# Performance work log

Hardware: AMD Instinct MI355X
Metric: run time of the kernel (lower is better)

## Reference

```python
import jax, jax.numpy as jnp
import numpy as np

NG, NT, E = 2500, 20000, 640000
SRC_DIM, DST_DIM, HID, OUT, NCLS = 128, 500, 128, 128, 16


def setup_inputs() -> dict:
    key = jax.random.key(0)
    ks = jax.random.split(key, 11)
    d = {
        "gene_feats": jax.random.normal(ks[0], (NG, SRC_DIM), jnp.float32),
        "train_feats": jax.random.normal(ks[1], (NT, DST_DIM), jnp.float32),
        "edge_src": jax.random.randint(ks[2], (E,), 0, NG),
        "edge_dst": jax.random.randint(ks[3], (E,), 0, NT),
        # conv1: SAGEConv((src_dim, dst_dim) -> hidden)
        "W1_neigh": jax.random.normal(ks[4], (SRC_DIM, HID), jnp.float32) / np.sqrt(SRC_DIM),
        "W1_self": jax.random.normal(ks[5], (DST_DIM, HID), jnp.float32) / np.sqrt(DST_DIM),
        "b1": jnp.zeros((HID,), jnp.float32),
        # conv2: SAGEConv(hidden -> out); src input is the raw gene features
        "W2_neigh": jax.random.normal(ks[6], (HID, OUT), jnp.float32) / np.sqrt(HID),
        "W2_self": jax.random.normal(ks[7], (HID, OUT), jnp.float32) / np.sqrt(HID),
        "b2": jnp.zeros((OUT,), jnp.float32),
        # classifier MLP
        "Wc1": jax.random.normal(ks[8], (OUT, OUT), jnp.float32) / np.sqrt(OUT),
        "bc1": jnp.zeros((OUT,), jnp.float32),
        "Wc2": jax.random.normal(ks[9], (OUT, NCLS), jnp.float32) / np.sqrt(OUT),
        "bc2": jnp.zeros((NCLS,), jnp.float32),
    }
    return d


def _segment_mean(msgs, dst, num_segments):
    # mean over in-edges; isolated dst nodes get 0 (DGL convention)
    sums = jax.ops.segment_sum(msgs, dst, num_segments=num_segments)
    cnt = jax.ops.segment_sum(jnp.ones((msgs.shape[0],), msgs.dtype), dst,
                              num_segments=num_segments)
    return sums / jnp.maximum(cnt, 1.0)[:, None]


def reference(gene_feats, train_feats, edge_src, edge_dst,
              W1_neigh, W1_self, b1, W2_neigh, W2_self, b2,
              Wc1, bc1, Wc2, bc2):
    # mean-aggregate gene (src) features onto train (dst) nodes
    agg = _segment_mean(gene_feats[edge_src], edge_dst, NT)  # [NT, SRC_DIM]
    # conv1: fc_self(h_dst) + fc_neigh(mean_neigh) + bias, then ReLU
    h1 = jax.nn.relu(train_feats @ W1_self + agg @ W1_neigh + b1)  # [NT, HID]
    # conv2 reuses raw gene features as src -> same mean aggregation
    h2 = jax.nn.relu(h1 @ W2_self + agg @ W2_neigh + b2)  # [NT, OUT]
    # classifier: Linear -> ReLU -> Linear
    return jax.nn.relu(h2 @ Wc1 + bc1) @ Wc2 + bc2  # [NT, NCLS]
```

## Files before the change

### kernel.cpp

```cpp
#include <hip/hip_runtime.h>


#define NG 2500
#define NT 20000
#define NE 640000
#define NCLS 16
#define CAP 96
#define NTILE 1250

typedef unsigned short u16;
typedef unsigned int u32;

typedef float f32x4 __attribute__((ext_vector_type(4)));
typedef __bf16 bf16x8 __attribute__((ext_vector_type(8)));

__device__ __forceinline__ float b2f(u16 u) { return __uint_as_float(((u32)u) << 16); }
__device__ __forceinline__ float blo(u32 p) { return __uint_as_float(p << 16); }
__device__ __forceinline__ float bhi(u32 p) { return __uint_as_float(p & 0xffff0000u); }
__device__ __forceinline__ u16 f2b(float f) {
    u32 u = __float_as_uint(f);
    return (u16)((u + 0x7fffu + ((u >> 16) & 1u)) >> 16);
}

#define B1N 81920
#define B2N 32768
#define B3N 16384
#define B4N 2048
#define NEB 2500
#define CVB NTILE
#define GNB 625
#define PKB 520

__global__ __launch_bounds__(256) void k_prep(
    const int* __restrict__ esrc, const int* __restrict__ edst,
    int* __restrict__ cnt, u16* __restrict__ csr,
    const float* __restrict__ train, const float* __restrict__ gene,
    u16* __restrict__ AF, u32* __restrict__ GH32,
    const float* __restrict__ W1n, const float* __restrict__ W1s,
    const float* __restrict__ W2n, const float* __restrict__ W2s,
    const float* __restrict__ Wc1, const float* __restrict__ Wc2,
    u16* __restrict__ B1h, u16* __restrict__ B1l,
    u16* __restrict__ B2h, u16* __restrict__ B2l,
    u16* __restrict__ B3h, u16* __restrict__ B3l,
    u16* __restrict__ B4h, u16* __restrict__ B4l) {
    int blk = blockIdx.x, t = threadIdx.x;
    if (blk < NEB) {
        int e = blk * 256 + t;
        if (e < NE) {
            unsigned d = (unsigned)edst[e];
            if (d < NT) {
                int slot = atomicAdd(&cnt[d], 1);
                if (slot < CAP) csr[(size_t)d * CAP + slot] = (u16)esrc[e];
            }
        }
        return;
    }
    if (blk < NEB + CVB) {
        __shared__ __align__(16) u16 L[16 * 520];
        u32* L32 = (u32*)L;
        int tile = blk - NEB;
        for (int i = t; i < 160; i += 256) {
            int r = i / 10, c = i - r * 10;
            L32[r * 260 + 250 + c] = 0;
        }
        for (int i = t; i < 2000; i += 256) {
            int r = i / 125, c4 = i - r * 125;
            float4 v = *(const float4*)(train + (size_t)(tile * 16 + r) * 500 + c4 * 4);
            int base = r * 260 + c4 * 2;
            L32[base] = (u32)f2b(v.x) | ((u32)f2b(v.y) << 16);
            L32[base + 1] = (u32)f2b(v.z) | ((u32)f2b(v.w) << 16);
        }
        __syncthreads();
#pragma unroll
        for (int it = 0; it < 4; ++it) {
            int slot = t + it * 256;
            int kk = slot >> 6, lane = slot & 63;
            int m = lane & 15, q = lane >> 4;
            uint4 v = *(const uint4*)(L + m * 520 + kk * 32 + q * 8);
            *(uint4*)(AF + (((size_t)tile * 16 + kk) * 64 + lane) * 8) = v;
        }
        return;
    }
    if (blk < NEB + CVB + GNB) {
        int idx = (blk - NEB - CVB) * 256 + t;
        float2 v = ((const float2*)gene)[idx];
        GH32[idx] = (u32)f2b(v.x) | ((u32)f2b(v.y) << 16);
        return;
    }
    int idx = (blk - NEB - CVB - GNB) * 256 + t;
    float v = 0.f;
    u16 *ph = 0, *pl = 0;
    int off = 0;
    if (idx < B1N) {
        int j = idx & 7, l = (idx >> 3) & 63, rest = idx >> 9;
        int g = rest & 7, kk = rest >> 3;
        int k = kk * 32 + ((l >> 4) << 3) + j, n = (g << 4) + (l & 15);
        if (k < 500) v = W1s[k * 128 + n];
        else if (k >= 512) v = W1n[(k - 512) * 128 + n];
        ph = B1h; pl = B1l; off = idx;
    } else if (idx < B1N + B2N) {
        int e = idx - B1N;
        int j = e & 7, l = (e >> 3) & 63, rest = e >> 9;
        int g = rest & 7, kk = rest >> 3;
        int k = kk * 32 + ((l >> 4) << 3) + j, n = (g << 4) + (l & 15);
        v = (k < 128) ? W2s[k * 128 + n] : W2n[(k - 128) * 128 + n];
        ph = B2h; pl = B2l; off = e;
    } else if (idx < B1N + B2N + B3N) {
        int e = idx - (B1N + B2N);
        int j = e & 7, l = (e >> 3) & 63, rest = e >> 9;
        int g = rest & 7, kk = rest >> 3;
        int k = kk * 32 + ((l >> 4) << 3) + j, n = (g << 4) + (l & 15);
        v = Wc1[k * 128 + n];
        ph = B3h; pl = B3l; off = e;
    } else if (idx < B1N + B2N + B3N + B4N) {
        int e = idx - (B1N + B2N + B3N);
        int j = e & 7, l = (e >> 3) & 63, kk = e >> 9;
        int k = kk * 32 + ((l >> 4) << 3) + j, n = l & 15;
        v = Wc2[k * 16 + n];
        ph = B4h; pl = B4l; off = e;
    }
    if (ph) {
        u16 hi = f2b(v);
        u16 lo = f2b(v - b2f(hi));
        ph[off] = hi;
        pl[off] = lo;
    }
}

__global__ __launch_bounds__(512) void k_mega(
    const int* __restrict__ cnt, const u16* __restrict__ csr,
    const u16* __restrict__ GH, const u16* __restrict__ AF,
    const u16* __restrict__ B1h, const u16* __restrict__ B1l,
    const u16* __restrict__ B2h, const u16* __restrict__ B2l,
    const u16* __restrict__ B3h, const u16* __restrict__ B3l,
    const u16* __restrict__ B4h, const u16* __restrict__ B4l,
    const float* __restrict__ b1, const float* __restrict__ b2,
    const float* __restrict__ bc1, const float* __restrict__ bc2,
    float* __restrict__ out) {
    __shared__ __align__(16) u16 SAGh[32 * 136], SAGl[32 * 136];
    __shared__ __align__(16) u16 S1h[32 * 136], S1l[32 * 136];
    __shared__ __align__(16) u16 S2h[32 * 136], S2l[32 * 136];
    int t = threadIdx.x;
    int row0 = blockIdx.x * 32;

    {
        int r = t >> 4, cg = t & 15;
        int d = row0 + r;
        int ctrue = cnt[d];
        int c = ctrue > CAP ? CAP : ctrue;
        const u16* crow = csr + (size_t)d * CAP;
        float a[8];
#pragma unroll
        for (int p = 0; p < 8; ++p) a[p] = 0.f;
        int j = 0;
        for (; j + 1 < c; j += 2) {
            int s0 = crow[j], s1 = crow[j + 1];
            uint4 p0 = *(const uint4*)(GH + (size_t)s0 * 128 + cg * 8);
            uint4 p1 = *(const uint4*)(GH + (size_t)s1 * 128 + cg * 8);
            a[0] += blo(p0.x); a[1] += bhi(p0.x);
            a[2] += blo(p0.y); a[3] += bhi(p0.y);
            a[4] += blo(p0.z); a[5] += bhi(p0.z);
            a[6] += blo(p0.w); a[7] += bhi(p0.w);
            a[0] += blo(p1.x); a[1] += bhi(p1.x);
            a[2] += blo(p1.y); a[3] += bhi(p1.y);
            a[4] += blo(p1.z); a[5] += bhi(p1.z);
            a[6] += blo(p1.w); a[7] += bhi(p1.w);
        }
        if (j < c) {
            int s = crow[j];
            uint4 p0 = *(const uint4*)(GH + (size_t)s * 128 + cg * 8);
            a[0] += blo(p0.x); a[1] += bhi(p0.x);
            a[2] += blo(p0.y); a[3] += bhi(p0.y);
            a[4] += blo(p0.z); a[5] += bhi(p0.z);
            a[6] += blo(p0.w); a[7] += bhi(p0.w);
        }
        float inv = (ctrue > 0) ? 1.f / (float)ctrue : 0.f;
        int base = (r * 136 + cg * 8) >> 1;
        u32* SH = (u32*)SAGh;
        u32* SL = (u32*)SAGl;
#pragma unroll
        for (int p = 0; p < 4; ++p) {
            float x = a[2 * p] * inv, y = a[2 * p + 1] * inv;
            u16 hx = f2b(x), hy = f2b(y);
            SH[base + p] = (u32)hx | ((u32)hy << 16);
            SL[base + p] = (u32)f2b(x - b2f(hx)) | ((u32)f2b(y - b2f(hy)) << 16);
        }
    }
    __syncthreads();

    int lane = t & 63, g = t >> 6;
    int m = lane & 15, q = lane >> 4, n16 = lane & 15;
    size_t tile0 = (size_t)blockIdx.x * 2;

    const u16* aB0 = AF + ((tile0 * 16) * 64 + lane) * 8;
    const u16* aB1 = AF + (((tile0 + 1) * 16) * 64 + lane) * 8;
    int hr0 = m * 136 + q * 8;
    int hr1 = (16 + m) * 136 + q * 8;
    int cr0 = q * 4, cr1 = 16 + q * 4;
    const f32x4 z4 = {0.f, 0.f, 0.f, 0.f};
    f32x4 acc0 = z4, acc1 = z4;

#pragma unroll 4
    for (int kk = 0; kk < 16; ++kk) {
        bf16x8 a0 = *(const bf16x8*)(aB0 + kk * 512);
        bf16x8 a1 = *(const bf16x8*)(aB1 + kk * 512);
        size_t bo = ((size_t)(kk * 8 + g) * 64 + lane) * 8;
        bf16x8 bh = *(const bf16x8*)(B1h + bo);
        bf16x8 bl = *(const bf16x8*)(B1l + bo);
        acc0 = __builtin_amdgcn_mfma_f32_16x16x32_bf16(a0, bh, acc0, 0, 0, 0);
        acc0 = __builtin_amdgcn_mfma_f32_16x16x32_bf16(a0, bl, acc0, 0, 0, 0);
        acc1 = __builtin_amdgcn_mfma_f32_16x16x32_bf16(a1, bh, acc1, 0, 0, 0);
        acc1 = __builtin_amdgcn_mfma_f32_16x16x32_bf16(a1, bl, acc1, 0, 0, 0);
    }
#pragma unroll
    for (int kk = 16; kk < 20; ++kk) {
        int o = (kk - 16) * 32;
        bf16x8 ah0 = *(const bf16x8*)(SAGh + hr0 + o);
        bf16x8 al0 = *(const bf16x8*)(SAGl + hr0 + o);
        bf16x8 ah1 = *(const bf16x8*)(SAGh + hr1 + o);
        bf16x8 al1 = *(const bf16x8*)(SAGl + hr1 + o);
        size_t bo = ((size_t)(kk * 8 + g) * 64 + lane) * 8;
        bf16x8 bh = *(const bf16x8*)(B1h + bo);
        bf16x8 bl = *(const bf16x8*)(B1l + bo);
        acc0 = __builtin_amdgcn_mfma_f32_16x16x32_bf16(ah0, bh, acc0, 0, 0, 0);
        acc0 = __builtin_amdgcn_mfma_f32_16x16x32_bf16(ah0, bl, acc0, 0, 0, 0);
        acc0 = __builtin_amdgcn_mfma_f32_16x16x32_bf16(al0, bh, acc0, 0, 0, 0);
        acc1 = __builtin_amdgcn_mfma_f32_16x16x32_bf16(ah1, bh, acc1, 0, 0, 0);
        acc1 = __builtin_amdgcn_mfma_f32_16x16x32_bf16(ah1, bl, acc1, 0, 0, 0);
        acc1 = __builtin_amdgcn_mfma_f32_16x16x32_bf16(al1, bh, acc1, 0, 0, 0);
    }
    {
        int n = g * 16 + n16;
        float bias = b1[n];
#pragma unroll
        for (int rg = 0; rg < 4; ++rg) {
            float v0 = acc0[rg] + bias; v0 = v0 > 0.f ? v0 : 0.f;
            float v1 = acc1[rg] + bias; v1 = v1 > 0.f ? v1 : 0.f;
            u16 h0 = f2b(v0), h1v = f2b(v1);
            S1h[(cr0 + rg) * 136 + n] = h0; S1l[(cr0 + rg) * 136 + n] = f2b(v0 - b2f(h0));
            S1h[(cr1 + rg) * 136 + n] = h1v; S1l[(cr1 + rg) * 136 + n] = f2b(v1 - b2f(h1v));
        }
    }
    __syncthreads();

    acc0 = z4; acc1 = z4;
#pragma unroll
    for (int kk = 0; kk < 8; ++kk) {
        const u16* Ph = (kk < 4) ? S1h : SAGh;
        const u16* Pl = (kk < 4) ? S1l : SAGl;
        int o = (kk & 3) * 32;
        bf16x8 ah0 = *(const bf16x8*)(Ph + hr0 + o);
        bf16x8 al0 = *(const bf16x8*)(Pl + hr0 + o);
        bf16x8 ah1 = *(const bf16x8*)(Ph + hr1 + o);
        bf16x8 al1 = *(const bf16x8*)(Pl + hr1 + o);
        size_t bo = ((size_t)(kk * 8 + g) * 64 + lane) * 8;
        bf16x8 bh = *(const bf16x8*)(B2h + bo);
        bf16x8 bl = *(const bf16x8*)(B2l + bo);
        acc0 = __builtin_amdgcn_mfma_f32_16x16x32_bf16(ah0, bh, acc0, 0, 0, 0);
        acc0 = __builtin_amdgcn_mfma_f32_16x16x32_bf16(ah0, bl, acc0, 0, 0, 0);
        acc0 = __builtin_amdgcn_mfma_f32_16x16x32_bf16(al0, bh, acc0, 0, 0, 0);
        acc1 = __builtin_amdgcn_mfma_f32_16x16x32_bf16(ah1, bh, acc1, 0, 0, 0);
        acc1 = __builtin_amdgcn_mfma_f32_16x16x32_bf16(ah1, bl, acc1, 0, 0, 0);
        acc1 = __builtin_amdgcn_mfma_f32_16x16x32_bf16(al1, bh, acc1, 0, 0, 0);
    }
    {
        int n = g * 16 + n16;
        float bias = b2[n];
#pragma unroll
        for (int rg = 0; rg < 4; ++rg) {
            float v0 = acc0[rg] + bias; v0 = v0 > 0.f ? v0 : 0.f;
            float v1 = acc1[rg] + bias; v1 = v1 > 0.f ? v1 : 0.f;
            u16 h0 = f2b(v0), h1v = f2b(v1);
            S2h[(cr0 + rg) * 136 + n] = h0; S2l[(cr0 + rg) * 136 + n] = f2b(v0 - b2f(h0));
            S2h[(cr1 + rg) * 136 + n] = h1v; S2l[(cr1 + rg) * 136 + n] = f2b(v1 - b2f(h1v));
        }
    }
    __syncthreads();

    acc0 = z4; acc1 = z4;
#pragma unroll
    for (int kk = 0; kk < 4; ++kk) {
        int o = kk * 32;
        bf16x8 ah0 = *(const bf16x8*)(S2h + hr0 + o);
        bf16x8 al0 = *(const bf16x8*)(S2l + hr0 + o);
        bf16x8 ah1 = *(const bf16x8*)(S2h + hr1 + o);
        bf16x8 al1 = *(const bf16x8*)(S2l + hr1 + o);
        size_t bo = ((size_t)(kk * 8 + g) * 64 + lane) * 8;
        bf16x8 bh = *(const bf16x8*)(B3h + bo);
        bf16x8 bl = *(const bf16x8*)(B3l + bo);
        acc0 = __builtin_amdgcn_mfma_f32_16x16x32_bf16(ah0, bh, acc0, 0, 0, 0);
        acc0 = __builtin_amdgcn_mfma_f32_16x16x32_bf16(ah0, bl, acc0, 0, 0, 0);
        acc0 = __builtin_amdgcn_mfma_f32_16x16x32_bf16(al0, bh, acc0, 0, 0, 0);
        acc1 = __builtin_amdgcn_mfma_f32_16x16x32_bf16(ah1, bh, acc1, 0, 0, 0);
        acc1 = __builtin_amdgcn_mfma_f32_16x16x32_bf16(ah1, bl, acc1, 0, 0, 0);
        acc1 = __builtin_amdgcn_mfma_f32_16x16x32_bf16(al1, bh, acc1, 0, 0, 0);
    }
    {
        int n = g * 16 + n16;
        float bias = bc1[n];
#pragma unroll
        for (int rg = 0; rg < 4; ++rg) {
            float v0 = acc0[rg] + bias; v0 = v0 > 0.f ? v0 : 0.f;
            float v1 = acc1[rg] + bias; v1 = v1 > 0.f ? v1 : 0.f;
            u16 h0 = f2b(v0), h1v = f2b(v1);
            S1h[(cr0 + rg) * 136 + n] = h0; S1l[(cr0 + rg) * 136 + n] = f2b(v0 - b2f(h0));
            S1h[(cr1 + rg) * 136 + n] = h1v; S1l[(cr1 + rg) * 136 + n] = f2b(v1 - b2f(h1v));
        }
    }
    __syncthreads();

    if (g < 2) {
        int hr = (g == 0) ? hr0 : hr1;
        int cr = (g == 0) ? cr0 : cr1;
        f32x4 a4 = z4;
#pragma unroll
        for (int kk = 0; kk < 4; ++kk) {
            bf16x8 ah = *(const bf16x8*)(S1h + hr + kk * 32);
            bf16x8 al = *(const bf16x8*)(S1l + hr + kk * 32);
            size_t bo = ((size_t)kk * 64 + lane) * 8;
            bf16x8 bh = *(const bf16x8*)(B4h + bo);
            bf16x8 bl = *(const bf16x8*)(B4l + bo);
            a4 = __builtin_amdgcn_mfma_f32_16x16x32_bf16(ah, bh, a4, 0, 0, 0);
            a4 = __builtin_amdgcn_mfma_f32_16x16x32_bf16(ah, bl, a4, 0, 0, 0);
            a4 = __builtin_amdgcn_mfma_f32_16x16x32_bf16(al, bh, a4, 0, 0, 0);
        }
        float bias = bc2[n16];
#pragma unroll
        for (int rg = 0; rg < 4; ++rg)
            out[(size_t)(row0 + cr + rg) * NCLS + n16] = a4[rg] + bias;
    }
}

extern "C" void kernel_launch(void* const* d_in, const int* in_sizes, int n_in,
                              void* d_out, int out_size, void* d_ws, size_t ws_size,
                              hipStream_t stream) {
    const float* gene = (const float*)d_in[0];
    const float* train = (const float*)d_in[1];
    const int* esrc = (const int*)d_in[2];
    const int* edst = (const int*)d_in[3];

    char* ws = (char*)d_ws;
    int* cnt = (int*)(ws + 0);
    u16* csr = (u16*)(ws + 80000);
    u16* AF = (u16*)(ws + 3920000);
    u16* GH = (u16*)(ws + 24400000);
    u16* B1h = (u16*)(ws + 25040000);
    u16* B1l = (u16*)(ws + 25203840);
    u16* B2h = (u16*)(ws + 25367680);
    u16* B2l = (u16*)(ws + 25433216);
    u16* B3h = (u16*)(ws + 25498752);
    u16* B3l = (u16*)(ws + 25531520);
    u16* B4h = (u16*)(ws + 25564288);
    u16* B4l = (u16*)(ws + 25568384);

    hipMemsetAsync(cnt, 0, NT * sizeof(int), stream);
    k_prep<<<NEB + CVB + GNB + PKB, 256, 0, stream>>>(
        esrc, edst, cnt, csr, train, gene, AF, (u32*)GH,
        (const float*)d_in[4], (const float*)d_in[5], (const float*)d_in[7],
        (const float*)d_in[8], (const float*)d_in[10], (const float*)d_in[12],
        B1h, B1l, B2h, B2l, B3h, B3l, B4h, B4l);
    k_mega<<<NT / 32, 512, 0, stream>>>(
        cnt, csr, GH, AF, B1h, B1l, B2h, B2l, B3h, B3l, B4h, B4l,
        (const float*)d_in[6], (const float*)d_in[9], (const float*)d_in[11],
        (const float*)d_in[13], (float*)d_out);
}
```

Measured before the change: 183.3 us.

## Fuse train-feature bf16 conversion into main kernel and vectorize edge binning

Drops the prep pass that converted train_feats to a bf16 MFMA-fragment buffer in workspace. The main kernel now loads fp32 train rows directly, packs them to bf16 in registers and feeds the first-layer MFMA. The last K chunk clamps its addresses and relies on the zero-padded weight rows for columns 500-511. This removes one full write and read of the converted activation buffer, though the fused loads are less regular per lane. Separately, the edge-binning blocks now handle four edges per thread using int4 loads, which cuts the block count.

```diff
diff --git a/kernel.cpp b/kernel.cpp
--- a/kernel.cpp
+++ b/kernel.cpp
@@ -6,7 +6,6 @@
 #define NE 640000
 #define NCLS 16
 #define CAP 96
-#define NTILE 1250
 
 typedef unsigned short u16;
 typedef unsigned int u32;
@@ -22,20 +21,25 @@
     return (u16)((u + 0x7fffu + ((u >> 16) & 1u)) >> 16);
 }
 
+__device__ __forceinline__ bf16x8 pack8(float4 a, float4 b) {
+    bf16x8 r;
+    r[0] = (__bf16)a.x; r[1] = (__bf16)a.y; r[2] = (__bf16)a.z; r[3] = (__bf16)a.w;
+    r[4] = (__bf16)b.x; r[5] = (__bf16)b.y; r[6] = (__bf16)b.z; r[7] = (__bf16)b.w;
+    return r;
+}
+
 #define B1N 81920
 #define B2N 32768
 #define B3N 16384
 #define B4N 2048
-#define NEB 2500
-#define CVB NTILE
+#define NEB 625
 #define GNB 625
 #define PKB 520
 
 __global__ __launch_bounds__(256) void k_prep(
     const int* __restrict__ esrc, const int* __restrict__ edst,
     int* __restrict__ cnt, u16* __restrict__ csr,
-    const float* __restrict__ train, const float* __restrict__ gene,
-    u16* __restrict__ AF, u32* __restrict__ GH32,
+    const float* __restrict__ gene, u32* __restrict__ GH32,
     const float* __restrict__ W1n, const float* __restrict__ W1s,
     const float* __restrict__ W2n, const float* __restrict__ W2s,
     const float* __restrict__ Wc1, const float* __restrict__ Wc2,
@@ -45,49 +49,28 @@
     u16* __restrict__ B4h, u16* __restrict__ B4l) {
     int blk = blockIdx.x, t = threadIdx.x;
     if (blk < NEB) {
-        int e = blk * 256 + t;
-        if (e < NE) {
-            unsigned d = (unsigned)edst[e];
+        int e0 = (blk * 256 + t) * 4;
+        const int4 s4 = *(const int4*)(esrc + e0);
+        const int4 d4 = *(const int4*)(edst + e0);
+        int ss[4] = {s4.x, s4.y, s4.z, s4.w};
+        int dd[4] = {d4.x, d4.y, d4.z, d4.w};
+#pragma unroll
+        for (int i = 0; i < 4; ++i) {
+            unsigned d = (unsigned)dd[i];
             if (d < NT) {
                 int slot = atomicAdd(&cnt[d], 1);
-                if (slot < CAP) csr[(size_t)d * CAP + slot] = (u16)esrc[e];
+                if (slot < CAP) csr[(size_t)d * CAP + slot] = (u16)ss[i];
             }
         }
         return;
     }
-    if (blk < NEB + CVB) {
-        __shared__ __align__(16) u16 L[16 * 520];
-        u32* L32 = (u32*)L;
-        int tile = blk - NEB;
-        for (int i = t; i < 160; i += 256) {
-            int r = i / 10, c = i - r * 10;
-            L32[r * 260 + 250 + c] = 0;
-        }
-        for (int i = t; i < 2000; i += 256) {
-            int r = i / 125, c4 = i - r * 125;
-            float4 v = *(const float4*)(train + (size_t)(tile * 16 + r) * 500 + c4 * 4);
-            int base = r * 260 + c4 * 2;
-            L32[base] = (u32)f2b(v.x) | ((u32)f2b(v.y) << 16);
-            L32[base + 1] = (u32)f2b(v.z) | ((u32)f2b(v.w) << 16);
-        }
-        __syncthreads();
-#pragma unroll
-        for (int it = 0; it < 4; ++it) {
-            int slot = t + it * 256;
-            int kk = slot >> 6, lane = slot & 63;
-            int m = lane & 15, q = lane >> 4;
-            uint4 v = *(const uint4*)(L + m * 520 + kk * 32 + q * 8);
-            *(uint4*)(AF + (((size_t)tile * 16 + kk) * 64 + lane) * 8) = v;
-        }
-        return;
-    }
-    if (blk < NEB + CVB + GNB) {
-        int idx = (blk - NEB - CVB) * 256 + t;
+    if (blk < NEB + GNB) {
+        int idx = (blk - NEB) * 256 + t;
         float2 v = ((const float2*)gene)[idx];
         GH32[idx] = (u32)f2b(v.x) | ((u32)f2b(v.y) << 16);
         return;
     }
-    int idx = (blk - NEB - CVB - GNB) * 256 + t;
+    int idx = (blk - NEB - GNB) * 256 + t;
     float v = 0.f;
     u16 *ph = 0, *pl = 0;
     int off = 0;
@@ -129,7 +112,7 @@
 
 __global__ __launch_bounds__(512) void k_mega(
     const int* __restrict__ cnt, const u16* __restrict__ csr,
-    const u16* __restrict__ GH, const u16* __restrict__ AF,
+    const u16* __restrict__ GH, const float* __restrict__ train,
     const u16* __restrict__ B1h, const u16* __restrict__ B1l,
     const u16* __restrict__ B2h, const u16* __restrict__ B2l,
     const u16* __restrict__ B3h, const u16* __restrict__ B3l,
@@ -190,23 +173,49 @@
 
     int lane = t & 63, g = t >> 6;
     int m = lane & 15, q = lane >> 4, n16 = lane & 15;
-    size_t tile0 = (size_t)blockIdx.x * 2;
-
-    const u16* aB0 = AF + ((tile0 * 16) * 64 + lane) * 8;
-    const u16* aB1 = AF + (((tile0 + 1) * 16) * 64 + lane) * 8;
+
     int hr0 = m * 136 + q * 8;
     int hr1 = (16 + m) * 136 + q * 8;
     int cr0 = q * 4, cr1 = 16 + q * 4;
     const f32x4 z4 = {0.f, 0.f, 0.f, 0.f};
     f32x4 acc0 = z4, acc1 = z4;
 
+    const float* tp0 = train + (size_t)(row0 + m) * 500 + q * 8;
+    const float* tp1 = tp0 + 16 * 500;
 #pragma unroll 4
-    for (int kk = 0; kk < 16; ++kk) {
-        bf16x8 a0 = *(const bf16x8*)(aB0 + kk * 512);
-        bf16x8 a1 = *(const bf16x8*)(aB1 + kk * 512);
+    for (int kk = 0; kk < 15; ++kk) {
+        float4 u0 = *(const float4*)(tp0 + kk * 32);
+        float4 u1 = *(const float4*)(tp0 + kk * 32 + 4);
+        float4 w0 = *(const float4*)(tp1 + kk * 32);
+        float4 w1 = *(const float4*)(tp1 + kk * 32 + 4);
         size_t bo = ((size_t)(kk * 8 + g) * 64 + lane) * 8;
         bf16x8 bh = *(const bf16x8*)(B1h + bo);
         bf16x8 bl = *(const bf16x8*)(B1l + bo);
+        bf16x8 a0 = pack8(u0, u1);
+        bf16x8 a1 = pack8(w0, w1);
+        acc0 = __builtin_amdgcn_mfma_f32_16x16x32_bf16(a0, bh, acc0, 0, 0, 0);
+        acc0 = __builtin_amdgcn_mfma_f32_16x16x32_bf16(a0, bl, acc0, 0, 0, 0);
+        acc1 = __builtin_amdgcn_mfma_f32_16x16x32_bf16(a1, bh, acc1, 0, 0, 0);
+        acc1 = __builtin_amdgcn_mfma_f32_16x16x32_bf16(a1, bl, acc1, 0, 0, 0);
+    }
+    {
+        const u32 FMAX = (u32)NT * 500u - 4u;
+        u32 f0 = (u32)(row0 + m) * 500u + 480u + (u32)q * 8u;
+        u32 f1 = f0 + 4u;
+        u32 h0 = f0 + 8000u, h1 = h0 + 4u;
+        f0 = f0 > FMAX ? FMAX : f0;
+        f1 = f1 > FMAX ? FMAX : f1;
+        h0 = h0 > FMAX ? FMAX : h0;
+        h1 = h1 > FMAX ? FMAX : h1;
+        float4 u0 = *(const float4*)(train + f0);
+        float4 u1 = *(const float4*)(train + f1);
+        float4 w0 = *(const float4*)(train + h0);
+        float4 w1 = *(const float4*)(train + h1);
+        size_t bo = ((size_t)(15 * 8 + g) * 64 + lane) * 8;
+        bf16x8 bh = *(const bf16x8*)(B1h + bo);
+        bf16x8 bl = *(const bf16x8*)(B1l + bo);
+        bf16x8 a0 = pack8(u0, u1);
+        bf16x8 a1 = pack8(w0, w1);
         acc0 = __builtin_amdgcn_mfma_f32_16x16x32_bf16(a0, bh, acc0, 0, 0, 0);
         acc0 = __builtin_amdgcn_mfma_f32_16x16x32_bf16(a0, bl, acc0, 0, 0, 0);
         acc1 = __builtin_amdgcn_mfma_f32_16x16x32_bf16(a1, bh, acc1, 0, 0, 0);
@@ -342,25 +351,24 @@
     char* ws = (char*)d_ws;
     int* cnt = (int*)(ws + 0);
     u16* csr = (u16*)(ws + 80000);
-    u16* AF = (u16*)(ws + 3920000);
-    u16* GH = (u16*)(ws + 24400000);
-    u16* B1h = (u16*)(ws + 25040000);
-    u16* B1l = (u16*)(ws + 25203840);
-    u16* B2h = (u16*)(ws + 25367680);
-    u16* B2l = (u16*)(ws + 25433216);
-    u16* B3h = (u16*)(ws + 25498752);
-    u16* B3l = (u16*)(ws + 25531520);
-    u16* B4h = (u16*)(ws + 25564288);
-    u16* B4l = (u16*)(ws + 25568384);
+    u16* GH = (u16*)(ws + 3920000);
+    u16* B1h = (u16*)(ws + 4560000);
+    u16* B1l = (u16*)(ws + 4723840);
+    u16* B2h = (u16*)(ws + 4887680);
+    u16* B2l = (u16*)(ws + 4953216);
+    u16* B3h = (u16*)(ws + 5018752);
+    u16* B3l = (u16*)(ws + 5051520);
+    u16* B4h = (u16*)(ws + 5084288);
+    u16* B4l = (u16*)(ws + 5088384);
 
     hipMemsetAsync(cnt, 0, NT * sizeof(int), stream);
-    k_prep<<<NEB + CVB + GNB + PKB, 256, 0, stream>>>(
-        esrc, edst, cnt, csr, train, gene, AF, (u32*)GH,
+    k_prep<<<NEB + GNB + PKB, 256, 0, stream>>>(
+        esrc, edst, cnt, csr, gene, (u32*)GH,
         (const float*)d_in[4], (const float*)d_in[5], (const float*)d_in[7],
         (const float*)d_in[8], (const float*)d_in[10], (const float*)d_in[12],
         B1h, B1l, B2h, B2l, B3h, B3l, B4h, B4l);
     k_mega<<<NT / 32, 512, 0, stream>>>(
-        cnt, csr, GH, AF, B1h, B1l, B2h, B2l, B3h, B3l, B4h, B4l,
+        cnt, csr, GH, train, B1h, B1l, B2h, B2l, B3h, B3l, B4h, B4l,
         (const float*)d_in[6], (const float*)d_in[9], (const float*)d_in[11],
         (const float*)d_in[13], (float*)d_out);
 }
```

After: 196.9 us. 7.4% more time.
